# Optimization experiments

Hardware: AMD Instinct MI355X
Metric: run time of the kernel (lower is better)

Reference implementation:

```python
import jax, jax.numpy as jnp
import numpy as np

N_WIRES = 4
N_OPS = 50
B = 131072

# --- Fixed random gate sequence for tq.RandomLayer (default op set: RX, RY, RZ, CNOT) ---
_rng = np.random.RandomState(42)
RAND_GATES = []  # (kind, wires): kind 0=RX,1=RY,2=RZ,3=CNOT
for _ in range(N_OPS):
    k = int(_rng.randint(4))
    if k < 3:
        RAND_GATES.append((k, (int(_rng.randint(N_WIRES)),)))
    else:
        c, t = _rng.choice(N_WIRES, 2, replace=False)
        RAND_GATES.append((3, (int(c), int(t))))

# --- gate matrices (theta may be scalar or batched (B,)) ---
def rx_mat(t):
    c, s = jnp.cos(t / 2), jnp.sin(t / 2)
    return jnp.stack([jnp.stack([c + 0j, -1j * s], -1),
                      jnp.stack([-1j * s, c + 0j], -1)], -2).astype(jnp.complex64)

def ry_mat(t):
    c, s = jnp.cos(t / 2), jnp.sin(t / 2)
    return jnp.stack([jnp.stack([c, -s], -1),
                      jnp.stack([s, c], -1)], -2).astype(jnp.complex64)

def rz_mat(t):
    em = jnp.exp(-0.5j * t.astype(jnp.complex64))
    ep = jnp.exp(0.5j * t.astype(jnp.complex64))
    z = jnp.zeros_like(em)
    return jnp.stack([jnp.stack([em, z], -1),
                      jnp.stack([z, ep], -1)], -2).astype(jnp.complex64)

def crx_mat(t):
    c = jnp.cos(t / 2) + 0j
    s = -1j * jnp.sin(t / 2)
    U = jnp.eye(4, dtype=jnp.complex64)
    U = U.at[2, 2].set(c).at[3, 3].set(c).at[2, 3].set(s).at[3, 2].set(s)
    return U

H_MAT = (jnp.array([[1, 1], [1, -1]], jnp.complex64) / np.sqrt(2.0).astype(np.float32))
SX_MAT = 0.5 * jnp.array([[1 + 1j, 1 - 1j], [1 - 1j, 1 + 1j]], jnp.complex64)
CNOT_MAT = jnp.array([[1, 0, 0, 0], [0, 1, 0, 0], [0, 0, 0, 1], [0, 0, 1, 0]], jnp.complex64)

def apply_1q(state, U, wire):
    # state: (B,2,2,2,2); U: (2,2) or (B,2,2)
    ax = 1 + wire
    st = jnp.moveaxis(state, ax, -1)
    if U.ndim == 3:
        out = jnp.einsum('bij,b...j->b...i', U, st)
    else:
        out = jnp.einsum('ij,...j->...i', U, st)
    return jnp.moveaxis(out, -1, ax)

def apply_2q(state, U, w0, w1):
    # U: (4,4) acting on (w0, w1) with w0 the leading (control) wire
    a0, a1 = 1 + w0, 1 + w1
    st = jnp.moveaxis(state, (a0, a1), (-2, -1))
    sh = st.shape
    st = st.reshape(sh[:-2] + (4,))
    st = jnp.einsum('ij,...j->...i', U, st)
    st = st.reshape(sh)
    return jnp.moveaxis(st, (-2, -1), (a0, a1))

def _forward(features, rand_params, rx0, ry0, rz0, crx0, gamma, beta, W, b):
    bsz = features.shape[0]
    state = jnp.zeros((bsz, 16), jnp.complex64).at[:, 0].set(1.0).reshape(bsz, 2, 2, 2, 2)
    # --- GeneralEncoder '4x4_ryzxy': layers ry, rz, rx, ry over wires 0..3, 16 angles ---
    layer_fns = [ry_mat, rz_mat, rx_mat, ry_mat]
    for l in range(4):
        for w in range(4):
            state = apply_1q(state, layer_fns[l](features[:, 4 * l + w]), w)
    # --- RandomLayer (50 ops) ---
    p = 0
    for kind, wires in RAND_GATES:
        if kind == 0:
            state = apply_1q(state, rx_mat(rand_params[p]), wires[0]); p += 1
        elif kind == 1:
            state = apply_1q(state, ry_mat(rand_params[p]), wires[0]); p += 1
        elif kind == 2:
            state = apply_1q(state, rz_mat(rand_params[p]), wires[0]); p += 1
        else:
            state = apply_2q(state, CNOT_MAT, wires[0], wires[1])
    # --- trainable block ---
    state = apply_1q(state, rx_mat(rx0[0]), 0)
    state = apply_1q(state, ry_mat(ry0[0]), 1)
    state = apply_1q(state, rz_mat(rz0[0]), 3)
    state = apply_2q(state, crx_mat(crx0[0]), 0, 2)
    state = apply_1q(state, H_MAT, 3)
    state = apply_1q(state, SX_MAT, 2)
    state = apply_2q(state, CNOT_MAT, 3, 0)
    # --- MeasureAll PauliZ: <Z_w> per wire ---
    probs = (state.real ** 2 + state.imag ** 2).reshape(bsz, 16)
    bits = (jnp.arange(16)[:, None] >> jnp.arange(3, -1, -1)[None, :]) & 1  # (16,4), wire0=MSB
    signs = (1.0 - 2.0 * bits).astype(jnp.float32)
    ez = probs @ signs  # (B,4)
    # --- BatchNorm1d (training mode: batch stats, biased var) ---
    mu = ez.mean(0)
    var = ez.var(0)
    xh = (ez - mu) / jnp.sqrt(var + 1e-5)
    out = xh * gamma + beta
    # --- Linear(4,1) ---
    return out @ W.T + b

def setup_inputs() -> dict:
    key = jax.random.key(0)
    ks = jax.random.split(key, 8)
    two_pi = 2.0 * np.pi
    return {
        'features': jax.random.normal(ks[0], (B, 16), jnp.float32),
        'rand_params': jax.random.uniform(ks[1], (N_OPS,), jnp.float32, 0.0, two_pi),
        'rx0': jax.random.uniform(ks[2], (1,), jnp.float32, 0.0, two_pi),
        'ry0': jax.random.uniform(ks[3], (1,), jnp.float32, 0.0, two_pi),
        'rz0': jax.random.uniform(ks[4], (1,), jnp.float32, 0.0, two_pi),
        'crx0': jax.random.uniform(ks[5], (1,), jnp.float32, 0.0, two_pi),
        'gamma': jnp.ones((N_WIRES,), jnp.float32),
        'beta': jnp.zeros((N_WIRES,), jnp.float32),
        'W': jax.random.normal(ks[6], (1, N_WIRES), jnp.float32) * 0.5,
        'b': jnp.zeros((1,), jnp.float32),
    }

def reference(features, rand_params, rx0, ry0, rz0, crx0, gamma, beta, W, b):
    return _forward(features, rand_params, rx0, ry0, rz0, crx0, gamma, beta, W, b)
```

## Files before the change

kernel.cpp:

```cpp
#include <hip/hip_runtime.h>
#include <math.h>


struct CGates {
  int kind[64];
  int w0[64];
  int w1[64];
  int pidx[64];
  int ng;
};

constexpr unsigned int c_mt_next(unsigned int (&mt)[624], int& pos) {
  if (pos >= 624) {
    for (int i = 0; i < 624; ++i) {
      unsigned int y = (mt[i] & 0x80000000u) | (mt[(i + 1) % 624] & 0x7fffffffu);
      unsigned int v = mt[(i + 397) % 624] ^ (y >> 1);
      if (y & 1u) v ^= 0x9908b0dfu;
      mt[i] = v;
    }
    pos = 0;
  }
  unsigned int y = mt[pos++];
  y ^= y >> 11;
  y ^= (y << 7) & 0x9d2c5680u;
  y ^= (y << 15) & 0xefc60000u;
  y ^= y >> 18;
  return y;
}

constexpr CGates make_gates() {
  CGates gl{};
  unsigned int mt[624] = {};
  mt[0] = 42u;
  for (int i = 1; i < 624; ++i)
    mt[i] = 1812433253u * (mt[i - 1] ^ (mt[i - 1] >> 30)) + (unsigned int)i;
  int pos = 624;
  int ng = 0, p = 0;
  for (int op = 0; op < 50; ++op) {
    unsigned int k = c_mt_next(mt, pos) & 3u;
    if (k < 3u) {
      unsigned int w = c_mt_next(mt, pos) & 3u;
      gl.kind[ng] = (int)k; gl.w0[ng] = (int)w; gl.w1[ng] = 0;
      gl.pidx[ng] = p++;
      ++ng;
    } else {
      int arr[4] = {0, 1, 2, 3};
      { unsigned int j = c_mt_next(mt, pos) & 3u;
        int t = arr[3]; arr[3] = arr[j]; arr[j] = t; }
      { unsigned int j = c_mt_next(mt, pos) & 3u;
        while (j > 2u) j = c_mt_next(mt, pos) & 3u;
        int t = arr[2]; arr[2] = arr[j]; arr[j] = t; }
      { unsigned int j = c_mt_next(mt, pos) & 1u;
        int t = arr[1]; arr[1] = arr[j]; arr[j] = t; }
      gl.kind[ng] = 3; gl.w0[ng] = arr[0]; gl.w1[ng] = arr[1]; gl.pidx[ng] = -1;
      ++ng;
    }
  }
  gl.kind[ng] = 0; gl.w0[ng] = 0; gl.w1[ng] = 0; gl.pidx[ng] = -2; ++ng;
  gl.kind[ng] = 1; gl.w0[ng] = 1; gl.w1[ng] = 0; gl.pidx[ng] = -3; ++ng;
  gl.kind[ng] = 2; gl.w0[ng] = 3; gl.w1[ng] = 0; gl.pidx[ng] = -4; ++ng;
  gl.kind[ng] = 4; gl.w0[ng] = 0; gl.w1[ng] = 2; gl.pidx[ng] = -5; ++ng;
  gl.kind[ng] = 5; gl.w0[ng] = 3; gl.w1[ng] = 0; gl.pidx[ng] = -1; ++ng;
  gl.kind[ng] = 6; gl.w0[ng] = 2; gl.w1[ng] = 0; gl.pidx[ng] = -1; ++ng;
  gl.kind[ng] = 3; gl.w0[ng] = 3; gl.w1[ng] = 0; gl.pidx[ng] = -1; ++ng;
  gl.ng = ng;
  return gl;
}

inline constexpr CGates GL = make_gates();


template <int TB>
__device__ __forceinline__ void ap_rx(float (&sx)[16], float (&sy)[16],
                                      float c, float s) {
#pragma unroll
  for (int i = 0; i < 16; ++i) {
    if (i & TB) continue;
    const int j = i | TB;
    float ax = sx[i], ay = sy[i], bx = sx[j], by = sy[j];
    sx[i] = c * ax + s * by;  sy[i] = c * ay - s * bx;
    sx[j] = c * bx + s * ay;  sy[j] = c * by - s * ax;
  }
}

template <int TB>
__device__ __forceinline__ void ap_ry(float (&sx)[16], float (&sy)[16],
                                      float c, float s) {
#pragma unroll
  for (int i = 0; i < 16; ++i) {
    if (i & TB) continue;
    const int j = i | TB;
    float ax = sx[i], ay = sy[i], bx = sx[j], by = sy[j];
    sx[i] = c * ax - s * bx;  sy[i] = c * ay - s * by;
    sx[j] = s * ax + c * bx;  sy[j] = s * ay + c * by;
  }
}

template <int TB>
__device__ __forceinline__ void ap_rz(float (&sx)[16], float (&sy)[16],
                                      float c, float s) {
#pragma unroll
  for (int i = 0; i < 16; ++i) {
    if (i & TB) continue;
    const int j = i | TB;
    float ax = sx[i], ay = sy[i], bx = sx[j], by = sy[j];
    sx[i] = c * ax + s * ay;  sy[i] = c * ay - s * ax;
    sx[j] = c * bx - s * by;  sy[j] = c * by + s * bx;
  }
}

template <int TB>
__device__ __forceinline__ void ap_h(float (&sx)[16], float (&sy)[16]) {
  const float r = 0.70710678118654752f;
#pragma unroll
  for (int i = 0; i < 16; ++i) {
    if (i & TB) continue;
    const int j = i | TB;
    float ax = sx[i], ay = sy[i], bx = sx[j], by = sy[j];
    sx[i] = r * (ax + bx);  sy[i] = r * (ay + by);
    sx[j] = r * (ax - bx);  sy[j] = r * (ay - by);
  }
}

template <int TB>
__device__ __forceinline__ void ap_sxg(float (&sx)[16], float (&sy)[16]) {
#pragma unroll
  for (int i = 0; i < 16; ++i) {
    if (i & TB) continue;
    const int j = i | TB;
    float ax = sx[i], ay = sy[i], bx = sx[j], by = sy[j];
    sx[i] = 0.5f * (ax - ay + bx + by);  sy[i] = 0.5f * (ay + ax + by - bx);
    sx[j] = 0.5f * (ax + ay + bx - by);  sy[j] = 0.5f * (ay - ax + by + bx);
  }
}

template <int CB, int TB>
__device__ __forceinline__ void ap_cnot(float (&sx)[16], float (&sy)[16]) {
#pragma unroll
  for (int i = 0; i < 16; ++i) {
    if (!(i & CB) || (i & TB)) continue;
    const int j = i | TB;
    float tx = sx[i], ty = sy[i];
    sx[i] = sx[j]; sy[i] = sy[j];
    sx[j] = tx;    sy[j] = ty;
  }
}

template <int CB, int TB>
__device__ __forceinline__ void ap_crx(float (&sx)[16], float (&sy)[16],
                                       float c, float s) {
#pragma unroll
  for (int i = 0; i < 16; ++i) {
    if (!(i & CB) || (i & TB)) continue;
    const int j = i | TB;
    float ax = sx[i], ay = sy[i], bx = sx[j], by = sy[j];
    sx[i] = c * ax + s * by;  sy[i] = c * ay - s * bx;
    sx[j] = c * bx + s * ay;  sy[j] = c * by - s * ax;
  }
}

template <int G>
__device__ __forceinline__ void apply_gates(
    float (&sx)[16], float (&sy)[16], const float* __restrict__ rp,
    const float* __restrict__ rx0, const float* __restrict__ ry0,
    const float* __restrict__ rz0, const float* __restrict__ crx0) {
  if constexpr (G < GL.ng) {
    constexpr int kind = GL.kind[G];
    constexpr int TB0 = 8 >> GL.w0[G];
    constexpr int TB1 = 8 >> GL.w1[G];
    constexpr int pi = GL.pidx[G];
    float c = 0.f, s = 0.f;
    if constexpr (kind == 0 || kind == 1 || kind == 2 || kind == 4) {
      float th;
      if constexpr (pi >= 0)       th = rp[pi];
      else if constexpr (pi == -2) th = rx0[0];
      else if constexpr (pi == -3) th = ry0[0];
      else if constexpr (pi == -4) th = rz0[0];
      else                         th = crx0[0];
      __sincosf(0.5f * th, &s, &c);
    }
    if constexpr (kind == 0)      ap_rx<TB0>(sx, sy, c, s);
    else if constexpr (kind == 1) ap_ry<TB0>(sx, sy, c, s);
    else if constexpr (kind == 2) ap_rz<TB0>(sx, sy, c, s);
    else if constexpr (kind == 3) ap_cnot<TB0, TB1>(sx, sy);
    else if constexpr (kind == 4) ap_crx<TB0, TB1>(sx, sy, c, s);
    else if constexpr (kind == 5) ap_h<TB0>(sx, sy);
    else                          ap_sxg<TB0>(sx, sy);
    apply_gates<G + 1>(sx, sy, rp, rx0, ry0, rz0, crx0);
  }
}

__device__ __forceinline__ void phase1(const float* __restrict__ features,
                                       long long b, float (&t01x)[4],
                                       float (&t01y)[4], float (&t23x)[4],
                                       float (&t23y)[4]) {
  const float4* fp = (const float4*)(features + b * 16);
  float4 F0 = fp[0], F1 = fp[1], F2 = fp[2], F3 = fp[3];
  float L0[4] = {F0.x, F0.y, F0.z, F0.w};
  float L1[4] = {F1.x, F1.y, F1.z, F1.w};
  float L2[4] = {F2.x, F2.y, F2.z, F2.w};
  float L3[4] = {F3.x, F3.y, F3.z, F3.w};
  float vax[4], vay[4], vbx[4], vby[4];
#pragma unroll
  for (int w = 0; w < 4; ++w) {
    float s0, c0; __sincosf(0.5f * L0[w], &s0, &c0);
    float s1, c1; __sincosf(0.5f * L1[w], &s1, &c1);
    float s2, c2; __sincosf(0.5f * L2[w], &s2, &c2);
    float s3, c3; __sincosf(0.5f * L3[w], &s3, &c3);
    float ax = c0 * c1, ay = -c0 * s1;
    float bx = s0 * c1, by = s0 * s1;
    float a2x = c2 * ax + s2 * by, a2y = c2 * ay - s2 * bx;
    float b2x = s2 * ay + c2 * bx, b2y = -s2 * ax + c2 * by;
    vax[w] = c3 * a2x - s3 * b2x; vay[w] = c3 * a2y - s3 * b2y;
    vbx[w] = s3 * a2x + c3 * b2x; vby[w] = s3 * a2y + c3 * b2y;
  }
  t01x[0] = vax[0] * vax[1] - vay[0] * vay[1]; t01y[0] = vax[0] * vay[1] + vay[0] * vax[1];
  t01x[1] = vax[0] * vbx[1] - vay[0] * vby[1]; t01y[1] = vax[0] * vby[1] + vay[0] * vbx[1];
  t01x[2] = vbx[0] * vax[1] - vby[0] * vay[1]; t01y[2] = vbx[0] * vay[1] + vby[0] * vax[1];
  t01x[3] = vbx[0] * vbx[1] - vby[0] * vby[1]; t01y[3] = vbx[0] * vby[1] + vby[0] * vbx[1];
  t23x[0] = vax[2] * vax[3] - vay[2] * vay[3]; t23y[0] = vax[2] * vay[3] + vay[2] * vax[3];
  t23x[1] = vax[2] * vbx[3] - vay[2] * vby[3]; t23y[1] = vax[2] * vby[3] + vay[2] * vbx[3];
  t23x[2] = vbx[2] * vax[3] - vby[2] * vay[3]; t23y[2] = vbx[2] * vay[3] + vby[2] * vax[3];
  t23x[3] = vbx[2] * vbx[3] - vby[2] * vby[3]; t23y[3] = vbx[2] * vby[3] + vby[2] * vbx[3];
}

__device__ __forceinline__ void phase2(const float2* __restrict__ Uld,
                                       const float (&t01x)[4], const float (&t01y)[4],
                                       const float (&t23x)[4], const float (&t23y)[4],
                                       float (&ez)[4]) {
  float sx[16], sy[16];
#pragma unroll
  for (int i = 0; i < 16; ++i) {
    int a = i >> 2, c = i & 3;
    sx[i] = t01x[a] * t23x[c] - t01y[a] * t23y[c];
    sy[i] = t01x[a] * t23y[c] + t01y[a] * t23x[c];
  }
  float e0 = 0.f, e1 = 0.f, e2 = 0.f, e3 = 0.f;
#pragma unroll
  for (int i = 0; i < 16; ++i) {
    float ax = 0.f, ay = 0.f;
#pragma unroll
    for (int j = 0; j < 16; ++j) {
      float2 u = Uld[i * 16 + j];
      ax += u.x * sx[j] - u.y * sy[j];
      ay += u.x * sy[j] + u.y * sx[j];
    }
    float p = ax * ax + ay * ay;
    e0 += (i & 8) ? -p : p;
    e1 += (i & 4) ? -p : p;
    e2 += (i & 2) ? -p : p;
    e3 += (i & 1) ? -p : p;
  }
  ez[0] = e0; ez[1] = e1; ez[2] = e2; ez[3] = e3;
}

__global__ __launch_bounds__(256) void fused_main_kernel(
    const float* __restrict__ features, const float* __restrict__ rand_params,
    const float* __restrict__ rx0, const float* __restrict__ ry0,
    const float* __restrict__ rz0, const float* __restrict__ crx0,
    float* __restrict__ ez_out, float* __restrict__ partials,
    float2* __restrict__ Uws, int B, int useEz) {
  __shared__ float2 ldsU[256];
  __shared__ float wred[4][8];
  int tid = threadIdx.x;
  long long b = (long long)blockIdx.x * 256 + tid;
  bool valid = b < B;

  float t01x[4], t01y[4], t23x[4], t23y[4];
  if (valid) phase1(features, b, t01x, t01y, t23x, t23y);

  if (tid < 16) {
    float sx[16], sy[16];
#pragma unroll
    for (int i = 0; i < 16; ++i) { sx[i] = (i == tid) ? 1.f : 0.f; sy[i] = 0.f; }
    apply_gates<0>(sx, sy, rand_params, rx0, ry0, rz0, crx0);
#pragma unroll
    for (int i = 0; i < 16; ++i) {
      ldsU[i * 16 + tid] = make_float2(sx[i], sy[i]);
      if (!useEz && blockIdx.x == 0) Uws[i * 16 + tid] = make_float2(sx[i], sy[i]);
    }
  }
  __syncthreads();

  float ez[4] = {0.f, 0.f, 0.f, 0.f};
  if (valid) {
    phase2(ldsU, t01x, t01y, t23x, t23y, ez);
    if (useEz) ((float4*)ez_out)[b] = make_float4(ez[0], ez[1], ez[2], ez[3]);
  }
  float q[8] = {ez[0], ez[1], ez[2], ez[3],
                ez[0] * ez[0], ez[1] * ez[1], ez[2] * ez[2], ez[3] * ez[3]};
#pragma unroll
  for (int off = 32; off; off >>= 1)
#pragma unroll
    for (int k = 0; k < 8; ++k) q[k] += __shfl_down(q[k], off, 64);
  int lane = tid & 63, wv = tid >> 6;
  if (lane == 0)
#pragma unroll
    for (int k = 0; k < 8; ++k) wred[wv][k] = q[k];
  __syncthreads();
  if (tid == 0) {
#pragma unroll
    for (int k = 0; k < 8; ++k)
      partials[(size_t)blockIdx.x * 8 + k] =
          wred[0][k] + wred[1][k] + wred[2][k] + wred[3][k];
  }
}

__global__ __launch_bounds__(256) void out_kernel(
    const float* __restrict__ partials, int nblk,
    const float* __restrict__ gamma, const float* __restrict__ beta,
    const float* __restrict__ W, const float* __restrict__ bias,
    const float* __restrict__ ez_in, const float* __restrict__ features,
    const float2* __restrict__ Uws, float* __restrict__ out,
    int B, int useEz, float invB) {
  __shared__ float wred[4][8];
  __shared__ float coefs[5];
  __shared__ float2 ldsU[256];
  int tid = threadIdx.x;

  float q[8] = {0.f, 0.f, 0.f, 0.f, 0.f, 0.f, 0.f, 0.f};
  for (int idx = tid; idx < nblk; idx += 256) {
    const float4* p4 = (const float4*)(partials + (size_t)idx * 8);
    float4 A = p4[0], Bq = p4[1];
    q[0] += A.x;  q[1] += A.y;  q[2] += A.z;  q[3] += A.w;
    q[4] += Bq.x; q[5] += Bq.y; q[6] += Bq.z; q[7] += Bq.w;
  }
#pragma unroll
  for (int off = 32; off; off >>= 1)
#pragma unroll
    for (int k = 0; k < 8; ++k) q[k] += __shfl_down(q[k], off, 64);
  int lane = tid & 63, wv = tid >> 6;
  if (lane == 0)
#pragma unroll
    for (int k = 0; k < 8; ++k) wred[wv][k] = q[k];
  if (!useEz) ldsU[tid] = Uws[tid];
  __syncthreads();
  if (tid == 0) {
    float c0 = bias[0];
#pragma unroll
    for (int w = 0; w < 4; ++w) {
      float Sw = wred[0][w] + wred[1][w] + wred[2][w] + wred[3][w];
      float Qw = wred[0][4 + w] + wred[1][4 + w] + wred[2][4 + w] + wred[3][4 + w];
      float mu = Sw * invB;
      float var = Qw * invB - mu * mu;
      float inv = rsqrtf(var + 1e-5f);
      coefs[w] = W[w] * gamma[w] * inv;
      c0 += W[w] * (beta[w] - gamma[w] * mu * inv);
    }
    coefs[4] = c0;
  }
  __syncthreads();

  long long b = (long long)blockIdx.x * 256 + tid;
  if (b >= B) return;
  float ez[4];
  if (useEz) {
    float4 e = ((const float4*)ez_in)[b];
    ez[0] = e.x; ez[1] = e.y; ez[2] = e.z; ez[3] = e.w;
  } else {
    float t01x[4], t01y[4], t23x[4], t23y[4];
    phase1(features, b, t01x, t01y, t23x, t23y);
    phase2(ldsU, t01x, t01y, t23x, t23y, ez);
  }
  out[b] = coefs[4] + coefs[0] * ez[0] + coefs[1] * ez[1] +
           coefs[2] * ez[2] + coefs[3] * ez[3];
}

extern "C" void kernel_launch(void* const* d_in, const int* in_sizes, int n_in,
                              void* d_out, int out_size, void* d_ws, size_t ws_size,
                              hipStream_t stream) {
  const float* features    = (const float*)d_in[0];
  const float* rand_params = (const float*)d_in[1];
  const float* rx0         = (const float*)d_in[2];
  const float* ry0         = (const float*)d_in[3];
  const float* rz0         = (const float*)d_in[4];
  const float* crx0        = (const float*)d_in[5];
  const float* gamma       = (const float*)d_in[6];
  const float* beta        = (const float*)d_in[7];
  const float* W           = (const float*)d_in[8];
  const float* bias        = (const float*)d_in[9];
  float* out = (float*)d_out;

  int B = in_sizes[0] / 16;
  int nblk = (B + 255) / 256;

  char* ws = (char*)d_ws;
  float* partials = (float*)ws;
  size_t u_off = ((size_t)nblk * 32 + 255) & ~(size_t)255;
  float2* Uws = (float2*)(ws + u_off);
  size_t ez_off = (u_off + 2048 + 255) & ~(size_t)255;
  float* ez = (float*)(ws + ez_off);
  int useEz = (ws_size >= ez_off + (size_t)B * 16) ? 1 : 0;

  fused_main_kernel<<<nblk, 256, 0, stream>>>(
      features, rand_params, rx0, ry0, rz0, crx0, ez, partials, Uws, B, useEz);
  out_kernel<<<nblk, 256, 0, stream>>>(
      partials, nblk, gamma, beta, W, bias, ez, features, Uws, out, B, useEz,
      1.0f / (float)B);
}
```

Baseline: 25.87 us.

## Fuse both kernels into one with atomic grid barrier and parallel unitary build

Replaces the two-kernel pipeline with a single kernel. Blocks accumulate batch-norm statistics through global atomics, then spin on a completion counter before applying the normalisation and linear layer, so the ez intermediate no longer goes through global memory. The gate chain is split into four chunks, each simulated by its own wavefront, and the four 16x16 partial unitaries are combined with LDS matrix products, which shortens the serial gate-simulation latency per block. The spin barrier relies on all 512 blocks being co-resident (launch_bounds with 2 blocks per CU) and adds a memset launch plus atomic contention.

```diff
diff --git a/kernel.cpp b/kernel.cpp
--- a/kernel.cpp
+++ b/kernel.cpp
@@ -69,6 +69,10 @@
 
 inline constexpr CGates GL = make_gates();
 
+inline constexpr int CK1 = GL.ng / 4;
+inline constexpr int CK2 = GL.ng / 2;
+inline constexpr int CK3 = (3 * GL.ng) / 4;
+
 
 template <int TB>
 __device__ __forceinline__ void ap_rx(float (&sx)[16], float (&sy)[16],
@@ -159,12 +163,12 @@
   }
 }
 
-template <int G>
-__device__ __forceinline__ void apply_gates(
+template <int G, int GEND>
+__device__ __forceinline__ void apply_range(
     float (&sx)[16], float (&sy)[16], const float* __restrict__ rp,
     const float* __restrict__ rx0, const float* __restrict__ ry0,
     const float* __restrict__ rz0, const float* __restrict__ crx0) {
-  if constexpr (G < GL.ng) {
+  if constexpr (G < GEND) {
     constexpr int kind = GL.kind[G];
     constexpr int TB0 = 8 >> GL.w0[G];
     constexpr int TB1 = 8 >> GL.w1[G];
@@ -186,7 +190,7 @@
     else if constexpr (kind == 4) ap_crx<TB0, TB1>(sx, sy, c, s);
     else if constexpr (kind == 5) ap_h<TB0>(sx, sy);
     else                          ap_sxg<TB0>(sx, sy);
-    apply_gates<G + 1>(sx, sy, rp, rx0, ry0, rz0, crx0);
+    apply_range<G + 1, GEND>(sx, sy, rp, rx0, ry0, rz0, crx0);
   }
 }
 
@@ -254,14 +258,19 @@
   ez[0] = e0; ez[1] = e1; ez[2] = e2; ez[3] = e3;
 }
 
-__global__ __launch_bounds__(256) void fused_main_kernel(
+__global__ __launch_bounds__(256, 2) void mono_kernel(
     const float* __restrict__ features, const float* __restrict__ rand_params,
     const float* __restrict__ rx0, const float* __restrict__ ry0,
     const float* __restrict__ rz0, const float* __restrict__ crx0,
-    float* __restrict__ ez_out, float* __restrict__ partials,
-    float2* __restrict__ Uws, int B, int useEz) {
-  __shared__ float2 ldsU[256];
+    const float* __restrict__ gamma, const float* __restrict__ beta,
+    const float* __restrict__ W, const float* __restrict__ bias,
+    float* __restrict__ acc, float* __restrict__ out, int B, int nblk,
+    float invB) {
+  __shared__ float2 chunks[4][256];
+  __shared__ float2 comb[2][256];
   __shared__ float wred[4][8];
+  __shared__ float coefs[5];
+
   int tid = threadIdx.x;
   long long b = (long long)blockIdx.x * 256 + tid;
   bool valid = b < B;
@@ -269,80 +278,79 @@
   float t01x[4], t01y[4], t23x[4], t23y[4];
   if (valid) phase1(features, b, t01x, t01y, t23x, t23y);
 
-  if (tid < 16) {
+  int wv = tid >> 6, lane = tid & 63;
+  if (lane < 16) {
     float sx[16], sy[16];
 #pragma unroll
-    for (int i = 0; i < 16; ++i) { sx[i] = (i == tid) ? 1.f : 0.f; sy[i] = 0.f; }
-    apply_gates<0>(sx, sy, rand_params, rx0, ry0, rz0, crx0);
-#pragma unroll
-    for (int i = 0; i < 16; ++i) {
-      ldsU[i * 16 + tid] = make_float2(sx[i], sy[i]);
-      if (!useEz && blockIdx.x == 0) Uws[i * 16 + tid] = make_float2(sx[i], sy[i]);
-    }
+    for (int i = 0; i < 16; ++i) { sx[i] = (i == lane) ? 1.f : 0.f; sy[i] = 0.f; }
+    if (wv == 0)      apply_range<0,   CK1  >(sx, sy, rand_params, rx0, ry0, rz0, crx0);
+    else if (wv == 1) apply_range<CK1, CK2  >(sx, sy, rand_params, rx0, ry0, rz0, crx0);
+    else if (wv == 2) apply_range<CK2, CK3  >(sx, sy, rand_params, rx0, ry0, rz0, crx0);
+    else              apply_range<CK3, GL.ng>(sx, sy, rand_params, rx0, ry0, rz0, crx0);
+#pragma unroll
+    for (int i = 0; i < 16; ++i)
+      chunks[wv][i * 16 + lane] = make_float2(sx[i], sy[i]);
+  }
+  __syncthreads();
+
+  {
+    int r = tid >> 4, c = tid & 15;
+    float xr = 0.f, xi = 0.f, yr = 0.f, yi = 0.f;
+#pragma unroll
+    for (int k = 0; k < 16; ++k) {
+      float2 g1 = chunks[1][r * 16 + k], g0 = chunks[0][k * 16 + c];
+      xr += g1.x * g0.x - g1.y * g0.y;  xi += g1.x * g0.y + g1.y * g0.x;
+      float2 g3 = chunks[3][r * 16 + k], g2 = chunks[2][k * 16 + c];
+      yr += g3.x * g2.x - g3.y * g2.y;  yi += g3.x * g2.y + g3.y * g2.x;
+    }
+    comb[0][r * 16 + c] = make_float2(xr, xi);
+    comb[1][r * 16 + c] = make_float2(yr, yi);
+  }
+  __syncthreads();
+
+  {
+    int r = tid >> 4, c = tid & 15;
+    float ur = 0.f, ui = 0.f;
+#pragma unroll
+    for (int k = 0; k < 16; ++k) {
+      float2 a = comb[1][r * 16 + k], d = comb[0][k * 16 + c];
+      ur += a.x * d.x - a.y * d.y;
+      ui += a.x * d.y + a.y * d.x;
+    }
+    chunks[0][r * 16 + c] = make_float2(ur, ui);
   }
   __syncthreads();
 
   float ez[4] = {0.f, 0.f, 0.f, 0.f};
-  if (valid) {
-    phase2(ldsU, t01x, t01y, t23x, t23y, ez);
-    if (useEz) ((float4*)ez_out)[b] = make_float4(ez[0], ez[1], ez[2], ez[3]);
-  }
+  if (valid) phase2(&chunks[0][0], t01x, t01y, t23x, t23y, ez);
+
   float q[8] = {ez[0], ez[1], ez[2], ez[3],
                 ez[0] * ez[0], ez[1] * ez[1], ez[2] * ez[2], ez[3] * ez[3]};
 #pragma unroll
   for (int off = 32; off; off >>= 1)
 #pragma unroll
     for (int k = 0; k < 8; ++k) q[k] += __shfl_down(q[k], off, 64);
-  int lane = tid & 63, wv = tid >> 6;
-  if (lane == 0)
+  if ((tid & 63) == 0)
 #pragma unroll
     for (int k = 0; k < 8; ++k) wred[wv][k] = q[k];
   __syncthreads();
+
   if (tid == 0) {
+    unsigned int* cnt = (unsigned int*)(acc + 512);
 #pragma unroll
     for (int k = 0; k < 8; ++k)
-      partials[(size_t)blockIdx.x * 8 + k] =
-          wred[0][k] + wred[1][k] + wred[2][k] + wred[3][k];
-  }
-}
-
-__global__ __launch_bounds__(256) void out_kernel(
-    const float* __restrict__ partials, int nblk,
-    const float* __restrict__ gamma, const float* __restrict__ beta,
-    const float* __restrict__ W, const float* __restrict__ bias,
-    const float* __restrict__ ez_in, const float* __restrict__ features,
-    const float2* __restrict__ Uws, float* __restrict__ out,
-    int B, int useEz, float invB) {
-  __shared__ float wred[4][8];
-  __shared__ float coefs[5];
-  __shared__ float2 ldsU[256];
-  int tid = threadIdx.x;
-
-  float q[8] = {0.f, 0.f, 0.f, 0.f, 0.f, 0.f, 0.f, 0.f};
-  for (int idx = tid; idx < nblk; idx += 256) {
-    const float4* p4 = (const float4*)(partials + (size_t)idx * 8);
-    float4 A = p4[0], Bq = p4[1];
-    q[0] += A.x;  q[1] += A.y;  q[2] += A.z;  q[3] += A.w;
-    q[4] += Bq.x; q[5] += Bq.y; q[6] += Bq.z; q[7] += Bq.w;
-  }
-#pragma unroll
-  for (int off = 32; off; off >>= 1)
-#pragma unroll
-    for (int k = 0; k < 8; ++k) q[k] += __shfl_down(q[k], off, 64);
-  int lane = tid & 63, wv = tid >> 6;
-  if (lane == 0)
-#pragma unroll
-    for (int k = 0; k < 8; ++k) wred[wv][k] = q[k];
-  if (!useEz) ldsU[tid] = Uws[tid];
-  __syncthreads();
-  if (tid == 0) {
+      atomicAdd(&acc[k * 64], wred[0][k] + wred[1][k] + wred[2][k] + wred[3][k]);
+    __threadfence();
+    atomicAdd(cnt, 1u);
+    while (atomicAdd(cnt, 0u) < (unsigned int)nblk) { }
+    float S[8];
+#pragma unroll
+    for (int k = 0; k < 8; ++k) S[k] = atomicAdd(&acc[k * 64], 0.0f);
     float c0 = bias[0];
 #pragma unroll
     for (int w = 0; w < 4; ++w) {
-      float Sw = wred[0][w] + wred[1][w] + wred[2][w] + wred[3][w];
-      float Qw = wred[0][4 + w] + wred[1][4 + w] + wred[2][4 + w] + wred[3][4 + w];
-      float mu = Sw * invB;
-      float var = Qw * invB - mu * mu;
+      float mu = S[w] * invB;
+      float var = S[4 + w] * invB - mu * mu;
       float inv = rsqrtf(var + 1e-5f);
       coefs[w] = W[w] * gamma[w] * inv;
       c0 += W[w] * (beta[w] - gamma[w] * mu * inv);
@@ -351,19 +359,9 @@
   }
   __syncthreads();
 
-  long long b = (long long)blockIdx.x * 256 + tid;
-  if (b >= B) return;
-  float ez[4];
-  if (useEz) {
-    float4 e = ((const float4*)ez_in)[b];
-    ez[0] = e.x; ez[1] = e.y; ez[2] = e.z; ez[3] = e.w;
-  } else {
-    float t01x[4], t01y[4], t23x[4], t23y[4];
-    phase1(features, b, t01x, t01y, t23x, t23y);
-    phase2(ldsU, t01x, t01y, t23x, t23y, ez);
-  }
-  out[b] = coefs[4] + coefs[0] * ez[0] + coefs[1] * ez[1] +
-           coefs[2] * ez[2] + coefs[3] * ez[3];
+  if (valid)
+    out[b] = coefs[4] + coefs[0] * ez[0] + coefs[1] * ez[1] +
+             coefs[2] * ez[2] + coefs[3] * ez[3];
 }
 
 extern "C" void kernel_launch(void* const* d_in, const int* in_sizes, int n_in,
@@ -384,17 +382,10 @@
   int B = in_sizes[0] / 16;
   int nblk = (B + 255) / 256;
 
-  char* ws = (char*)d_ws;
-  float* partials = (float*)ws;
-  size_t u_off = ((size_t)nblk * 32 + 255) & ~(size_t)255;
-  float2* Uws = (float2*)(ws + u_off);
-  size_t ez_off = (u_off + 2048 + 255) & ~(size_t)255;
-  float* ez = (float*)(ws + ez_off);
-  int useEz = (ws_size >= ez_off + (size_t)B * 16) ? 1 : 0;
-
-  fused_main_kernel<<<nblk, 256, 0, stream>>>(
-      features, rand_params, rx0, ry0, rz0, crx0, ez, partials, Uws, B, useEz);
-  out_kernel<<<nblk, 256, 0, stream>>>(
-      partials, nblk, gamma, beta, W, bias, ez, features, Uws, out, B, useEz,
-      1.0f / (float)B);
-}
+  float* acc = (float*)d_ws;
+  hipMemsetAsync(d_ws, 0, 4096, stream);
+
+  mono_kernel<<<nblk, 256, 0, stream>>>(
+      features, rand_params, rx0, ry0, rz0, crx0, gamma, beta, W, bias,
+      acc, out, B, nblk, 1.0f / (float)B);
+}
```

After: 59.72 us. 131% more time.

## Build circuit unitary once in a separate kernel, splitting gates across four waves

Applied to the files above, without the earlier changes.

The 16x16 circuit unitary was rebuilt by 16 threads in every block of the main kernel, running a long serial chain of gates per block. It is now built once by a single-block kernel: four waves each apply a quarter of the gates, and the partial unitaries are combined with two 16x16 complex matrix multiplies in shared memory. The main kernel then only copies the precomputed unitary into LDS, and phase2 reads it as float4 so two entries come per load. The cost is an extra kernel launch with a serial dependency, plus small rounding differences from reassociating the gate product.

```diff
diff --git a/kernel.cpp b/kernel.cpp
--- a/kernel.cpp
+++ b/kernel.cpp
@@ -69,6 +69,10 @@
 
 inline constexpr CGates GL = make_gates();
 
+inline constexpr int CK1 = GL.ng / 4;
+inline constexpr int CK2 = GL.ng / 2;
+inline constexpr int CK3 = (3 * GL.ng) / 4;
+
 
 template <int TB>
 __device__ __forceinline__ void ap_rx(float (&sx)[16], float (&sy)[16],
@@ -159,12 +163,12 @@
   }
 }
 
-template <int G>
-__device__ __forceinline__ void apply_gates(
+template <int G, int GEND>
+__device__ __forceinline__ void apply_range(
     float (&sx)[16], float (&sy)[16], const float* __restrict__ rp,
     const float* __restrict__ rx0, const float* __restrict__ ry0,
     const float* __restrict__ rz0, const float* __restrict__ crx0) {
-  if constexpr (G < GL.ng) {
+  if constexpr (G < GEND) {
     constexpr int kind = GL.kind[G];
     constexpr int TB0 = 8 >> GL.w0[G];
     constexpr int TB1 = 8 >> GL.w1[G];
@@ -186,7 +190,7 @@
     else if constexpr (kind == 4) ap_crx<TB0, TB1>(sx, sy, c, s);
     else if constexpr (kind == 5) ap_h<TB0>(sx, sy);
     else                          ap_sxg<TB0>(sx, sy);
-    apply_gates<G + 1>(sx, sy, rp, rx0, ry0, rz0, crx0);
+    apply_range<G + 1, GEND>(sx, sy, rp, rx0, ry0, rz0, crx0);
   }
 }
 
@@ -224,7 +228,7 @@
   t23x[3] = vbx[2] * vbx[3] - vby[2] * vby[3]; t23y[3] = vbx[2] * vby[3] + vby[2] * vbx[3];
 }
 
-__device__ __forceinline__ void phase2(const float2* __restrict__ Uld,
+__device__ __forceinline__ void phase2(const float4* __restrict__ U4,
                                        const float (&t01x)[4], const float (&t01y)[4],
                                        const float (&t23x)[4], const float (&t23y)[4],
                                        float (&ez)[4]) {
@@ -240,10 +244,11 @@
   for (int i = 0; i < 16; ++i) {
     float ax = 0.f, ay = 0.f;
 #pragma unroll
-    for (int j = 0; j < 16; ++j) {
-      float2 u = Uld[i * 16 + j];
-      ax += u.x * sx[j] - u.y * sy[j];
-      ay += u.x * sy[j] + u.y * sx[j];
+    for (int j2 = 0; j2 < 8; ++j2) {
+      float4 u = U4[i * 8 + j2];
+      int j = 2 * j2;
+      ax += u.x * sx[j] - u.y * sy[j] + u.z * sx[j + 1] - u.w * sy[j + 1];
+      ay += u.x * sy[j] + u.y * sx[j] + u.z * sy[j + 1] + u.w * sx[j + 1];
     }
     float p = ax * ax + ay * ay;
     e0 += (i & 8) ? -p : p;
@@ -254,37 +259,74 @@
   ez[0] = e0; ez[1] = e1; ez[2] = e2; ez[3] = e3;
 }
 
-__global__ __launch_bounds__(256) void fused_main_kernel(
-    const float* __restrict__ features, const float* __restrict__ rand_params,
-    const float* __restrict__ rx0, const float* __restrict__ ry0,
-    const float* __restrict__ rz0, const float* __restrict__ crx0,
-    float* __restrict__ ez_out, float* __restrict__ partials,
-    float2* __restrict__ Uws, int B, int useEz) {
+__global__ __launch_bounds__(256) void build_u_kernel(
+    const float* __restrict__ rand_params, const float* __restrict__ rx0,
+    const float* __restrict__ ry0, const float* __restrict__ rz0,
+    const float* __restrict__ crx0, float2* __restrict__ U_out) {
+  __shared__ float2 chunks[4][256];
+  __shared__ float2 comb[2][256];
+  int tid = threadIdx.x;
+  int wv = tid >> 6, lane = tid & 63;
+
+  if (lane < 16) {
+    float sx[16], sy[16];
+#pragma unroll
+    for (int i = 0; i < 16; ++i) { sx[i] = (i == lane) ? 1.f : 0.f; sy[i] = 0.f; }
+    if (wv == 0)      apply_range<0,   CK1  >(sx, sy, rand_params, rx0, ry0, rz0, crx0);
+    else if (wv == 1) apply_range<CK1, CK2  >(sx, sy, rand_params, rx0, ry0, rz0, crx0);
+    else if (wv == 2) apply_range<CK2, CK3  >(sx, sy, rand_params, rx0, ry0, rz0, crx0);
+    else              apply_range<CK3, GL.ng>(sx, sy, rand_params, rx0, ry0, rz0, crx0);
+#pragma unroll
+    for (int i = 0; i < 16; ++i)
+      chunks[wv][i * 16 + lane] = make_float2(sx[i], sy[i]);
+  }
+  __syncthreads();
+
+  {
+    int r = tid >> 4, c = tid & 15;
+    float xr = 0.f, xi = 0.f, yr = 0.f, yi = 0.f;
+#pragma unroll
+    for (int k = 0; k < 16; ++k) {
+      float2 g1 = chunks[1][r * 16 + k], g0 = chunks[0][k * 16 + c];
+      xr += g1.x * g0.x - g1.y * g0.y;  xi += g1.x * g0.y + g1.y * g0.x;
+      float2 g3 = chunks[3][r * 16 + k], g2 = chunks[2][k * 16 + c];
+      yr += g3.x * g2.x - g3.y * g2.y;  yi += g3.x * g2.y + g3.y * g2.x;
+    }
+    comb[0][r * 16 + c] = make_float2(xr, xi);
+    comb[1][r * 16 + c] = make_float2(yr, yi);
+  }
+  __syncthreads();
+
+  {
+    int r = tid >> 4, c = tid & 15;
+    float ur = 0.f, ui = 0.f;
+#pragma unroll
+    for (int k = 0; k < 16; ++k) {
+      float2 a = comb[1][r * 16 + k], d = comb[0][k * 16 + c];
+      ur += a.x * d.x - a.y * d.y;
+      ui += a.x * d.y + a.y * d.x;
+    }
+    U_out[r * 16 + c] = make_float2(ur, ui);
+  }
+}
+
+__global__ __launch_bounds__(256) void main_kernel(
+    const float* __restrict__ features, const float2* __restrict__ U,
+    float* __restrict__ ez_out, float* __restrict__ partials, int B, int useEz) {
   __shared__ float2 ldsU[256];
   __shared__ float wred[4][8];
   int tid = threadIdx.x;
+  ldsU[tid] = U[tid];
+
   long long b = (long long)blockIdx.x * 256 + tid;
   bool valid = b < B;
-
   float t01x[4], t01y[4], t23x[4], t23y[4];
   if (valid) phase1(features, b, t01x, t01y, t23x, t23y);
-
-  if (tid < 16) {
-    float sx[16], sy[16];
-#pragma unroll
-    for (int i = 0; i < 16; ++i) { sx[i] = (i == tid) ? 1.f : 0.f; sy[i] = 0.f; }
-    apply_gates<0>(sx, sy, rand_params, rx0, ry0, rz0, crx0);
-#pragma unroll
-    for (int i = 0; i < 16; ++i) {
-      ldsU[i * 16 + tid] = make_float2(sx[i], sy[i]);
-      if (!useEz && blockIdx.x == 0) Uws[i * 16 + tid] = make_float2(sx[i], sy[i]);
-    }
-  }
   __syncthreads();
 
   float ez[4] = {0.f, 0.f, 0.f, 0.f};
   if (valid) {
-    phase2(ldsU, t01x, t01y, t23x, t23y, ez);
+    phase2((const float4*)ldsU, t01x, t01y, t23x, t23y, ez);
     if (useEz) ((float4*)ez_out)[b] = make_float4(ez[0], ez[1], ez[2], ez[3]);
   }
   float q[8] = {ez[0], ez[1], ez[2], ez[3],
@@ -311,7 +353,7 @@
     const float* __restrict__ gamma, const float* __restrict__ beta,
     const float* __restrict__ W, const float* __restrict__ bias,
     const float* __restrict__ ez_in, const float* __restrict__ features,
-    const float2* __restrict__ Uws, float* __restrict__ out,
+    const float2* __restrict__ U, float* __restrict__ out,
     int B, int useEz, float invB) {
   __shared__ float wred[4][8];
   __shared__ float coefs[5];
@@ -333,7 +375,7 @@
   if (lane == 0)
 #pragma unroll
     for (int k = 0; k < 8; ++k) wred[wv][k] = q[k];
-  if (!useEz) ldsU[tid] = Uws[tid];
+  if (!useEz) ldsU[tid] = U[tid];
   __syncthreads();
   if (tid == 0) {
     float c0 = bias[0];
@@ -360,7 +402,7 @@
   } else {
     float t01x[4], t01y[4], t23x[4], t23y[4];
     phase1(features, b, t01x, t01y, t23x, t23y);
-    phase2(ldsU, t01x, t01y, t23x, t23y, ez);
+    phase2((const float4*)ldsU, t01x, t01y, t23x, t23y, ez);
   }
   out[b] = coefs[4] + coefs[0] * ez[0] + coefs[1] * ez[1] +
            coefs[2] * ez[2] + coefs[3] * ez[3];
@@ -385,16 +427,15 @@
   int nblk = (B + 255) / 256;
 
   char* ws = (char*)d_ws;
-  float* partials = (float*)ws;
-  size_t u_off = ((size_t)nblk * 32 + 255) & ~(size_t)255;
-  float2* Uws = (float2*)(ws + u_off);
-  size_t ez_off = (u_off + 2048 + 255) & ~(size_t)255;
+  float2* U = (float2*)ws;
+  float* partials = (float*)(ws + 2048);
+  size_t ez_off = (2048 + (size_t)nblk * 32 + 255) & ~(size_t)255;
   float* ez = (float*)(ws + ez_off);
   int useEz = (ws_size >= ez_off + (size_t)B * 16) ? 1 : 0;
 
-  fused_main_kernel<<<nblk, 256, 0, stream>>>(
-      features, rand_params, rx0, ry0, rz0, crx0, ez, partials, Uws, B, useEz);
-  out_kernel<<<nblk, 256, 0, stream>>>(
-      partials, nblk, gamma, beta, W, bias, ez, features, Uws, out, B, useEz,
-      1.0f / (float)B);
-}
+  build_u_kernel<<<1, 256, 0, stream>>>(rand_params, rx0, ry0, rz0, crx0, U);
+  main_kernel<<<nblk, 256, 0, stream>>>(features, U, ez, partials, B, useEz);
+  out_kernel<<<nblk, 256, 0, stream>>>(partials, nblk, gamma, beta, W, bias,
+                                       ez, features, U, out, B, useEz,
+                                       1.0f / (float)B);
+}
```

After: 25.21 us. -2.6%, faster.
